# Kernel tuning notes

Measured on AMD Instinct MI355X. Metric: run time of the kernel, lower is better.

The kernel has to match this reference:

```python
import jax, jax.numpy as jnp
import numpy as np

N = 100000       # nodes
E = 1600000      # edges (avg degree 16)
IN_DIM = 128
HIDDEN = 128


def _glorot(key, shape):
    s = 1.0 / np.sqrt(shape[0])
    return jax.random.uniform(key, shape, minval=-s, maxval=s, dtype=jnp.float32)


def setup_inputs() -> dict:
    key = jax.random.key(0)
    ks = jax.random.split(key, 8)
    x = jax.random.normal(ks[0], (N, IN_DIM), dtype=jnp.float32)
    edge_index = jax.random.randint(ks[1], (2, E), 0, N, dtype=jnp.int32)
    W0 = _glorot(ks[2], (IN_DIM, HIDDEN))
    b0 = jnp.zeros((HIDDEN,), dtype=jnp.float32)
    W1 = _glorot(ks[3], (HIDDEN, HIDDEN))
    b1 = jnp.zeros((HIDDEN,), dtype=jnp.float32)
    W2 = _glorot(ks[4], (HIDDEN, HIDDEN))
    b2 = jnp.zeros((HIDDEN,), dtype=jnp.float32)
    return {"x": x, "edge_index": edge_index,
            "W0": W0, "b0": b0, "W1": W1, "b1": b1, "W2": W2, "b2": b2}


def _gcn_conv(x, row, col, norm, W, b):
    # x' = W x, then out[i] = sum_{j in N(i) U {i}} norm_ji * x'[j], + bias
    h = x @ W                              # [N, out]
    msg = norm[:, None] * h[row]           # [E+N, out] gather + scale
    out = jax.ops.segment_sum(msg, col, num_segments=N)  # scatter-add
    return out + b


def reference(x, edge_index, W0, b0, W1, b1, W2, b2):
    # PyG GCNConv default: add self-loops, symmetric normalization D^-1/2 A D^-1/2
    self_loops = jnp.arange(N, dtype=edge_index.dtype)
    row = jnp.concatenate([edge_index[0], self_loops])  # sources
    col = jnp.concatenate([edge_index[1], self_loops])  # destinations
    deg = jax.ops.segment_sum(jnp.ones_like(col, dtype=x.dtype), col, num_segments=N)
    dinv = jax.lax.rsqrt(deg)              # deg >= 1 thanks to self-loops
    norm = dinv[row] * dinv[col]           # [E+N]

    h = _gcn_conv(x, row, col, norm, W0, b0)
    h = jax.nn.relu(h)                     # dropout: eval mode (identity)
    h = _gcn_conv(h, row, col, norm, W1, b1)
    h = jax.nn.relu(h)
    return _gcn_conv(h, row, col, norm, W2, b2)
```

## Files before the change

### kernel.cpp

```cpp
#include <hip/hip_runtime.h>

#define HID 128
#define BR  128
#define FILL_CHUNK 2048

typedef _Float16 f16;
typedef f16 f16x2 __attribute__((ext_vector_type(2)));
typedef f16 f16x4 __attribute__((ext_vector_type(4)));
typedef f16 f16x8 __attribute__((ext_vector_type(8)));
typedef float f32x4 __attribute__((ext_vector_type(4)));

static __device__ __forceinline__ float2 h2f(unsigned int u) {
    f16x2 v;
    __builtin_memcpy(&v, &u, 4);
    return make_float2((float)v[0], (float)v[1]);
}


__global__ void k_deg_count(const int* __restrict__ col, int* __restrict__ cnt8, int E, int N) {
    int* cnt = cnt8 + (size_t)(blockIdx.x & 7) * N;
    const int eend = min(E, (blockIdx.x + 1) * FILL_CHUNK);
    for (int e = blockIdx.x * FILL_CHUNK + threadIdx.x; e < eend; e += 256)
        atomicAdd(&cnt[__builtin_nontemporal_load(col + e)], 1);
}

__global__ void k_scan_block(const int* __restrict__ cnt8, int* __restrict__ excl,
                             int* __restrict__ bsum, float* __restrict__ dinv, int N) {
    __shared__ int s[256];
    int i = blockIdx.x * 256 + threadIdx.x;
    int v = 0;
    if (i < N) {
#pragma unroll
        for (int x = 0; x < 8; ++x) v += cnt8[(size_t)x * N + i];
        dinv[i] = 1.0f / sqrtf((float)(v + 1));
    }
    s[threadIdx.x] = v;
    __syncthreads();
    for (int off = 1; off < 256; off <<= 1) {
        int t = (threadIdx.x >= off) ? s[threadIdx.x - off] : 0;
        __syncthreads();
        s[threadIdx.x] += t;
        __syncthreads();
    }
    if (i < N) excl[i] = s[threadIdx.x] - v;
    if (threadIdx.x == 255) bsum[blockIdx.x] = s[255];
}

__global__ __launch_bounds__(1024) void k_scan_bsum(int* __restrict__ bsum, int nb) {
    __shared__ int s[1024];
    int i = threadIdx.x;
    int v = (i < nb) ? bsum[i] : 0;
    s[i] = v;
    __syncthreads();
    for (int off = 1; off < 1024; off <<= 1) {
        int t = (i >= off) ? s[i - off] : 0;
        __syncthreads();
        s[i] += t;
        __syncthreads();
    }
    if (i < nb) bsum[i] = s[i] - v;
}

__global__ void k_scan_add(int* __restrict__ row_ptr, const int* __restrict__ bsum,
                           int* __restrict__ fill, int N, int E) {
    int i = blockIdx.x * 256 + threadIdx.x;
    if (i < N) {
        int v = row_ptr[i] + bsum[blockIdx.x];
        row_ptr[i] = v;
        fill[i] = v;
    }
    if (i == 0) row_ptr[N] = E;
}

__global__ void k_fill(const int* __restrict__ row, const int* __restrict__ col,
                       int* __restrict__ fill, int* __restrict__ csr_src, int E, int N) {
    const int xcd = blockIdx.x & 7;
    const int chunk = blockIdx.x >> 3;
    const int per = (N + 7) >> 3;
    const int lo = xcd * per;
    const int hi = min(N, lo + per);
    const int eend = min(E, (chunk + 1) * FILL_CHUNK);
    for (int e = chunk * FILL_CHUNK + threadIdx.x; e < eend; e += 256) {
        int c = col[e];
        if (c >= lo && c < hi) {
            int p = atomicAdd(&fill[c], 1);
            csr_src[p] = row[e];
        }
    }
}


__global__ void k_wprep3(const float* __restrict__ W0, const float* __restrict__ W1,
                         const float* __restrict__ W2, f16* __restrict__ out) {
    const int b = blockIdx.x;
    const int which = b >> 4;
    const float* W = which == 0 ? W0 : (which == 1 ? W1 : W2);
    f16* o = out + which * 32768;
    int i = (b & 15) * 256 + threadIdx.x;
    int k = i >> 5, n0 = (i & 31) * 4;
    float4 v = reinterpret_cast<const float4*>(W)[i];
    float vv[4] = {v.x, v.y, v.z, v.w};
#pragma unroll
    for (int e = 0; e < 4; ++e) {
        int n = n0 + e;
        int idx = (k >> 3) * 1024 + n * 8 + (k & 7);
        f16 h = (f16)vv[e];
        o[idx] = h;
        o[16384 + idx] = (f16)(vv[e] - (float)h);
    }
}


template<int MODE>
__global__ __launch_bounds__(512, 4) void k_gemm(const void* __restrict__ Xv,
                                                 const f16* __restrict__ Wt,
                                                 const float* __restrict__ dinv,
                                                 f16* __restrict__ H, int N) {
    __shared__ f16 Xs[16384];
    const int t = threadIdx.x;
    const int row0 = blockIdx.x * BR;

    const int w  = t >> 6;
    const int l  = t & 63;
    const int lg = l >> 4;
    const int li = l & 15;
    const int ng = w & 3;
    const int mg = w >> 2;

    f16x8 Wh[2][4], Wl[2][4];
#pragma unroll
    for (int nb = 0; nb < 2; ++nb) {
        const int ncol = (ng * 2 + nb) * 16 + li;
#pragma unroll
        for (int ks = 0; ks < 4; ++ks) {
            const int idx = (ks * 4 + lg) * 1024 + ncol * 8;
            Wh[nb][ks] = *reinterpret_cast<const f16x8*>(&Wt[idx]);
            Wl[nb][ks] = *reinterpret_cast<const f16x8*>(&Wt[16384 + idx]);
        }
    }

    if constexpr (MODE == 0) {
        const float* X = (const float*)Xv;
        for (int i = t; i < 4096; i += 512) {
            int r = i >> 5, q = i & 31;
            int gr = row0 + r;
            float4 v = make_float4(0.f, 0.f, 0.f, 0.f);
            if (gr < N) v = reinterpret_cast<const float4*>(X + (size_t)gr * HID)[q];
            int base = r * 128 + (((q >> 1) ^ (r & 7)) * 8) + (q & 1) * 4;
            *reinterpret_cast<f16x4*>(&Xs[base]) =
                (f16x4){(f16)v.x, (f16)v.y, (f16)v.z, (f16)v.w};
        }
    } else {
        const f16* src = (const f16*)Xv + (size_t)row0 * HID;
        for (int i = t; i < 2048; i += 512)
            *reinterpret_cast<f16x8*>(&Xs[i * 8]) = *reinterpret_cast<const f16x8*>(src + (size_t)i * 8);
    }
    __syncthreads();

    f32x4 acc[2][4];
#pragma unroll
    for (int nb = 0; nb < 2; ++nb)
#pragma unroll
        for (int mb = 0; mb < 4; ++mb) acc[nb][mb] = (f32x4){0.f, 0.f, 0.f, 0.f};

#pragma unroll
    for (int mb = 0; mb < 4; ++mb) {
        const int arow = mg * 64 + mb * 16 + li;
#pragma unroll
        for (int ks = 0; ks < 4; ++ks) {
            const int idx = arow * 128 + (((ks * 4 + lg) ^ (arow & 7)) * 8);
            f16x8 Xh = *reinterpret_cast<const f16x8*>(&Xs[idx]);
#pragma unroll
            for (int nb = 0; nb < 2; ++nb) {
                acc[nb][mb] = __builtin_amdgcn_mfma_f32_16x16x32_f16(Wh[nb][ks], Xh, acc[nb][mb], 0, 0, 0);
                acc[nb][mb] = __builtin_amdgcn_mfma_f32_16x16x32_f16(Wl[nb][ks], Xh, acc[nb][mb], 0, 0, 0);
            }
        }
    }

#pragma unroll
    for (int mb = 0; mb < 4; ++mb) {
        const int m = row0 + mg * 64 + mb * 16 + li;
        if (m < N) {
            const float d = dinv[m];
#pragma unroll
            for (int nb = 0; nb < 2; ++nb) {
                f16x4 o = {(f16)(acc[nb][mb][0] * d), (f16)(acc[nb][mb][1] * d),
                           (f16)(acc[nb][mb][2] * d), (f16)(acc[nb][mb][3] * d)};
                *reinterpret_cast<f16x4*>(&H[(size_t)m * HID + (ng * 2 + nb) * 16 + lg * 4]) = o;
            }
        }
    }
}


template<bool F16OUT>
__global__ __launch_bounds__(256) void k_agg_csr(const f16* __restrict__ h,
                                                 const int* __restrict__ csr_src,
                                                 const int* __restrict__ row_ptr,
                                                 const float* __restrict__ dinv,
                                                 const float* __restrict__ bias,
                                                 void* __restrict__ outv, int N) {
    const int node = blockIdx.x * 8 + (threadIdx.x >> 5);
    if (node >= N) return;
    const int l = threadIdx.x & 31;
    const uint2* h2 = reinterpret_cast<const uint2*>(h);

    uint2 us = h2[(size_t)node * 32 + l];
    float2 a0 = h2f(us.x), a1 = h2f(us.y);
    float acc0 = a0.x, acc1 = a0.y, acc2 = a1.x, acc3 = a1.y;

    int j = row_ptr[node];
    const int end = row_ptr[node + 1];

    for (; j + 8 <= end; j += 8) {
        int s0 = csr_src[j];
        int s1 = csr_src[j + 1];
        int s2 = csr_src[j + 2];
        int s3 = csr_src[j + 3];
        int s4 = csr_src[j + 4];
        int s5 = csr_src[j + 5];
        int s6 = csr_src[j + 6];
        int s7 = csr_src[j + 7];
        uint2 u0 = h2[(size_t)s0 * 32 + l];
        uint2 u1 = h2[(size_t)s1 * 32 + l];
        uint2 u2 = h2[(size_t)s2 * 32 + l];
        uint2 u3 = h2[(size_t)s3 * 32 + l];
        uint2 u4 = h2[(size_t)s4 * 32 + l];
        uint2 u5 = h2[(size_t)s5 * 32 + l];
        uint2 u6 = h2[(size_t)s6 * 32 + l];
        uint2 u7 = h2[(size_t)s7 * 32 + l];
        float2 v0 = h2f(u0.x), w0 = h2f(u0.y), v1 = h2f(u1.x), w1 = h2f(u1.y);
        float2 v2 = h2f(u2.x), w2 = h2f(u2.y), v3 = h2f(u3.x), w3 = h2f(u3.y);
        float2 v4 = h2f(u4.x), w4 = h2f(u4.y), v5 = h2f(u5.x), w5 = h2f(u5.y);
        float2 v6 = h2f(u6.x), w6 = h2f(u6.y), v7 = h2f(u7.x), w7 = h2f(u7.y);
        acc0 += ((v0.x + v1.x) + (v2.x + v3.x)) + ((v4.x + v5.x) + (v6.x + v7.x));
        acc1 += ((v0.y + v1.y) + (v2.y + v3.y)) + ((v4.y + v5.y) + (v6.y + v7.y));
        acc2 += ((w0.x + w1.x) + (w2.x + w3.x)) + ((w4.x + w5.x) + (w6.x + w7.x));
        acc3 += ((w0.y + w1.y) + (w2.y + w3.y)) + ((w4.y + w5.y) + (w6.y + w7.y));
    }
    for (; j < end; ++j) {
        uint2 u = h2[(size_t)csr_src[j] * 32 + l];
        float2 v = h2f(u.x), w = h2f(u.y);
        acc0 += v.x; acc1 += v.y; acc2 += w.x; acc3 += w.y;
    }

    const float di = dinv[node];
    const float4 bv = reinterpret_cast<const float4*>(bias)[l];
    float o0 = fmaf(di, acc0, bv.x);
    float o1 = fmaf(di, acc1, bv.y);
    float o2 = fmaf(di, acc2, bv.z);
    float o3 = fmaf(di, acc3, bv.w);

    if constexpr (F16OUT) {
        o0 = fmaxf(o0, 0.f); o1 = fmaxf(o1, 0.f);
        o2 = fmaxf(o2, 0.f); o3 = fmaxf(o3, 0.f);
        const int swz = (((l >> 1) ^ (node & 7)) << 1) | (l & 1);
        f16x4 o = {(f16)o0, (f16)o1, (f16)o2, (f16)o3};
        *reinterpret_cast<f16x4*>((f16*)outv + (size_t)node * HID + swz * 4) = o;
    } else {
        *reinterpret_cast<float4*>((float*)outv + (size_t)node * HID + l * 4) =
            make_float4(o0, o1, o2, o3);
    }
}


extern "C" void kernel_launch(void* const* d_in, const int* in_sizes, int n_in,
                              void* d_out, int out_size, void* d_ws, size_t ws_size,
                              hipStream_t stream) {
    const float* x  = (const float*)d_in[0];
    const int*   ei = (const int*)  d_in[1];
    const float* W0 = (const float*)d_in[2];
    const float* b0 = (const float*)d_in[3];
    const float* W1 = (const float*)d_in[4];
    const float* b1 = (const float*)d_in[5];
    const float* W2 = (const float*)d_in[6];
    const float* b2 = (const float*)d_in[7];

    const int N = in_sizes[0] / HID;
    const int E = in_sizes[1] / 2;
    const int* row = ei;
    const int* col = ei + E;

    const int nb_n = (N + 255) / 256;

    f16*   h16     = (f16*)d_ws;
    float* dinv    = (float*)(h16 + (size_t)N * HID);
    int*   cnt8    = (int*)(dinv + N);
    int*   row_ptr = cnt8 + (size_t)8 * N;
    int*   fill    = row_ptr + (N + 1);
    int*   bsum    = fill + N;
    int*   csr_src = bsum + nb_n;
    f16*   wt      = (f16*)(csr_src + E);
    f16*   wt0     = wt;
    f16*   wt1     = wt + 32768;
    f16*   wt2     = wt + 65536;
    f16*   act     = (f16*)d_out;
    float* out     = (float*)d_out;

    const int nb_gemm  = (N + BR - 1) / BR;
    const int nb_agg   = (N + 7) / 8;
    const int nb_chunk = (E + FILL_CHUNK - 1) / FILL_CHUNK;
    const int nb_fill  = nb_chunk * 8;

    (void)hipMemsetAsync(cnt8, 0, (size_t)8 * N * sizeof(int), stream);
    k_wprep3<<<48, 256, 0, stream>>>(W0, W1, W2, wt);
    k_deg_count <<<nb_chunk, 256, 0, stream>>>(col, cnt8, E, N);
    k_scan_block<<<nb_n, 256, 0, stream>>>(cnt8, row_ptr, bsum, dinv, N);
    k_scan_bsum <<<1, 1024, 0, stream>>>(bsum, nb_n);
    k_scan_add  <<<nb_n, 256, 0, stream>>>(row_ptr, bsum, fill, N, E);
    k_fill      <<<nb_fill, 256, 0, stream>>>(row, col, fill, csr_src, E, N);

    k_gemm<0>      <<<nb_gemm, 512, 0, stream>>>(x, wt0, dinv, h16, N);
    k_agg_csr<true><<<nb_agg, 256, 0, stream>>>(h16, csr_src, row_ptr, dinv, b0, act, N);
    k_gemm<1>      <<<nb_gemm, 512, 0, stream>>>(act, wt1, dinv, h16, N);
    k_agg_csr<true><<<nb_agg, 256, 0, stream>>>(h16, csr_src, row_ptr, dinv, b1, act, N);
    k_gemm<1>      <<<nb_gemm, 512, 0, stream>>>(act, wt2, dinv, h16, N);
    k_agg_csr<false><<<nb_agg, 256, 0, stream>>>(h16, csr_src, row_ptr, dinv, b2, out, N);
}
```

Before: 418.9 us.

## Fuse weight prep with degree count, halve fill windows, prefetch CSR indices

Merges the weight-conversion kernel into the degree-count kernel so one launch replaces two. Splits the CSR fill into four destination windows instead of eight, so each edge chunk is scanned by fewer blocks but each block does more atomics. Adds software prefetching of the next eight neighbor indices in the aggregation loop, so index loads overlap with feature gathers. The trade-off is more register use and a different contention pattern in the fill atomics.

Measured after the change: 412.1 us. Within noise of the previous version (-1.6%).

```diff
diff --git a/kernel.cpp b/kernel.cpp
--- a/kernel.cpp
+++ b/kernel.cpp
@@ -17,11 +17,34 @@
 }
 
 
-__global__ void k_deg_count(const int* __restrict__ col, int* __restrict__ cnt8, int E, int N) {
-    int* cnt = cnt8 + (size_t)(blockIdx.x & 7) * N;
-    const int eend = min(E, (blockIdx.x + 1) * FILL_CHUNK);
-    for (int e = blockIdx.x * FILL_CHUNK + threadIdx.x; e < eend; e += 256)
-        atomicAdd(&cnt[__builtin_nontemporal_load(col + e)], 1);
+__global__ void k_prep_count(const float* __restrict__ W0, const float* __restrict__ W1,
+                             const float* __restrict__ W2, f16* __restrict__ wt,
+                             const int* __restrict__ col, int* __restrict__ cnt8,
+                             int E, int N) {
+    if (blockIdx.x < 48) {
+        const int b = blockIdx.x;
+        const int which = b >> 4;
+        const float* W = which == 0 ? W0 : (which == 1 ? W1 : W2);
+        f16* o = wt + which * 32768;
+        int i = (b & 15) * 256 + threadIdx.x;
+        int k = i >> 5, n0 = (i & 31) * 4;
+        float4 v = reinterpret_cast<const float4*>(W)[i];
+        float vv[4] = {v.x, v.y, v.z, v.w};
+#pragma unroll
+        for (int e = 0; e < 4; ++e) {
+            int n = n0 + e;
+            int idx = (k >> 3) * 1024 + n * 8 + (k & 7);
+            f16 h = (f16)vv[e];
+            o[idx] = h;
+            o[16384 + idx] = (f16)(vv[e] - (float)h);
+        }
+    } else {
+        const int bb = blockIdx.x - 48;
+        int* cnt = cnt8 + (size_t)(bb & 7) * N;
+        const int eend = min(E, (bb + 1) * FILL_CHUNK);
+        for (int e = bb * FILL_CHUNK + threadIdx.x; e < eend; e += 256)
+            atomicAdd(&cnt[__builtin_nontemporal_load(col + e)], 1);
+    }
 }
 
 __global__ void k_scan_block(const int* __restrict__ cnt8, int* __restrict__ excl,
@@ -74,10 +97,10 @@
 
 __global__ void k_fill(const int* __restrict__ row, const int* __restrict__ col,
                        int* __restrict__ fill, int* __restrict__ csr_src, int E, int N) {
-    const int xcd = blockIdx.x & 7;
-    const int chunk = blockIdx.x >> 3;
-    const int per = (N + 7) >> 3;
-    const int lo = xcd * per;
+    const int win = blockIdx.x & 3;
+    const int chunk = blockIdx.x >> 2;
+    const int per = (N + 3) >> 2;
+    const int lo = win * per;
     const int hi = min(N, lo + per);
     const int eend = min(E, (chunk + 1) * FILL_CHUNK);
     for (int e = chunk * FILL_CHUNK + threadIdx.x; e < eend; e += 256) {
@@ -86,27 +109,6 @@
             int p = atomicAdd(&fill[c], 1);
             csr_src[p] = row[e];
         }
-    }
-}
-
-
-__global__ void k_wprep3(const float* __restrict__ W0, const float* __restrict__ W1,
-                         const float* __restrict__ W2, f16* __restrict__ out) {
-    const int b = blockIdx.x;
-    const int which = b >> 4;
-    const float* W = which == 0 ? W0 : (which == 1 ? W1 : W2);
-    f16* o = out + which * 32768;
-    int i = (b & 15) * 256 + threadIdx.x;
-    int k = i >> 5, n0 = (i & 31) * 4;
-    float4 v = reinterpret_cast<const float4*>(W)[i];
-    float vv[4] = {v.x, v.y, v.z, v.w};
-#pragma unroll
-    for (int e = 0; e < 4; ++e) {
-        int n = n0 + e;
-        int idx = (k >> 3) * 1024 + n * 8 + (k & 7);
-        f16 h = (f16)vv[e];
-        o[idx] = h;
-        o[16384 + idx] = (f16)(vv[e] - (float)h);
     }
 }
 
@@ -213,15 +215,24 @@
     int j = row_ptr[node];
     const int end = row_ptr[node + 1];
 
-    for (; j + 8 <= end; j += 8) {
-        int s0 = csr_src[j];
-        int s1 = csr_src[j + 1];
-        int s2 = csr_src[j + 2];
-        int s3 = csr_src[j + 3];
-        int s4 = csr_src[j + 4];
-        int s5 = csr_src[j + 5];
-        int s6 = csr_src[j + 6];
-        int s7 = csr_src[j + 7];
+    int s0, s1, s2, s3, s4, s5, s6, s7;
+    bool have = (j + 8 <= end);
+    if (have) {
+        s0 = csr_src[j];     s1 = csr_src[j + 1];
+        s2 = csr_src[j + 2]; s3 = csr_src[j + 3];
+        s4 = csr_src[j + 4]; s5 = csr_src[j + 5];
+        s6 = csr_src[j + 6]; s7 = csr_src[j + 7];
+    }
+    while (have) {
+        const int jn = j + 8;
+        const bool haven = (jn + 8 <= end);
+        int t0, t1, t2, t3, t4, t5, t6, t7;
+        if (haven) {
+            t0 = csr_src[jn];     t1 = csr_src[jn + 1];
+            t2 = csr_src[jn + 2]; t3 = csr_src[jn + 3];
+            t4 = csr_src[jn + 4]; t5 = csr_src[jn + 5];
+            t6 = csr_src[jn + 6]; t7 = csr_src[jn + 7];
+        }
         uint2 u0 = h2[(size_t)s0 * 32 + l];
         uint2 u1 = h2[(size_t)s1 * 32 + l];
         uint2 u2 = h2[(size_t)s2 * 32 + l];
@@ -238,6 +249,9 @@
         acc1 += ((v0.y + v1.y) + (v2.y + v3.y)) + ((v4.y + v5.y) + (v6.y + v7.y));
         acc2 += ((w0.x + w1.x) + (w2.x + w3.x)) + ((w4.x + w5.x) + (w6.x + w7.x));
         acc3 += ((w0.y + w1.y) + (w2.y + w3.y)) + ((w4.y + w5.y) + (w6.y + w7.y));
+        s0 = t0; s1 = t1; s2 = t2; s3 = t3; s4 = t4; s5 = t5; s6 = t6; s7 = t7;
+        j = jn;
+        have = haven;
     }
     for (; j < end; ++j) {
         uint2 u = h2[(size_t)csr_src[j] * 32 + l];
@@ -301,11 +315,10 @@
     const int nb_gemm  = (N + BR - 1) / BR;
     const int nb_agg   = (N + 7) / 8;
     const int nb_chunk = (E + FILL_CHUNK - 1) / FILL_CHUNK;
-    const int nb_fill  = nb_chunk * 8;
+    const int nb_fill  = nb_chunk * 4;
 
     (void)hipMemsetAsync(cnt8, 0, (size_t)8 * N * sizeof(int), stream);
-    k_wprep3<<<48, 256, 0, stream>>>(W0, W1, W2, wt);
-    k_deg_count <<<nb_chunk, 256, 0, stream>>>(col, cnt8, E, N);
+    k_prep_count<<<nb_chunk + 48, 256, 0, stream>>>(W0, W1, W2, wt, col, cnt8, E, N);
     k_scan_block<<<nb_n, 256, 0, stream>>>(cnt8, row_ptr, bsum, dinv, N);
     k_scan_bsum <<<1, 1024, 0, stream>>>(bsum, nb_n);
     k_scan_add  <<<nb_n, 256, 0, stream>>>(row_ptr, bsum, fill, N, E);
```
